# Performance work log

Measured on AMD Instinct MI355X. Metric: run time of the kernel, lower is better.

## Reference

```python
import jax, jax.numpy as jnp
import numpy as np

TOP_K = 2  # num_experts_per_tok


def setup_inputs() -> dict:
    key = jax.random.key(0)
    k1, k2, k3, k4, k5 = jax.random.split(key, 5)
    T, H, F, E = 2048, 2048, 1024, 8
    hidden_states = jax.random.normal(k1, (T, H), dtype=jnp.float32)
    router_logits = jax.random.normal(k2, (T, E), dtype=jnp.float32)
    s = 1.0 / np.sqrt(H)
    w1 = jax.random.normal(k3, (E, H, F), dtype=jnp.float32) * s  # gate proj
    w3 = jax.random.normal(k4, (E, H, F), dtype=jnp.float32) * s  # up proj
    w2 = jax.random.normal(k5, (E, F, H), dtype=jnp.float32) * (1.0 / np.sqrt(F))  # down proj
    return {"hidden_states": hidden_states, "router_logits": router_logits,
            "w1": w1, "w3": w3, "w2": w2}


def reference(hidden_states, router_logits, w1, w3, w2):
    # Top-K routing: softmax over raw logits, take top-k probs as combine weights
    # (renormalize_topk_logits=False, routed_scaling_factor=None).
    T, E = router_logits.shape
    probs = jax.nn.softmax(router_logits.astype(jnp.float32), axis=-1)  # (T, E)
    topk_w, topk_ids = jax.lax.top_k(probs, TOP_K)                      # (T, K)
    # Scatter combine weights into a dense (T, E) matrix (zeros off top-k).
    combine = jnp.zeros((T, E), dtype=probs.dtype).at[
        jnp.arange(T)[:, None], topk_ids].add(topk_w)                    # (T, E)

    x = hidden_states
    # SwiGLU expert FFN computed per-expert (dense over all tokens, masked by
    # combine weights -> same math as fused dispatch/grouped-GEMM/combine).
    g = jnp.einsum('th,ehf->etf', x, w1)          # (E, T, F) gate
    u = jnp.einsum('th,ehf->etf', x, w3)          # (E, T, F) up
    act = jax.nn.silu(g) * u                      # (E, T, F)
    act = act * combine.T[:, :, None]             # apply combine weight pre-down-proj
    y = jnp.einsum('etf,efh->th', act, w2)        # (T, H) combined over experts
    return y.astype(hidden_states.dtype)
```

## Files before the change

### kernel.cpp

```cpp
#include <hip/hip_runtime.h>
#include <stdint.h>

#define T_TOK 2048
#define HDIM  2048
#define FDIM  1024
#define NEXP  8

#define BM   128
#define BK   64
#define NTHR 256
#define MT_MAX 16
#define BN1  64
#define BN2  128
#define NT1 (FDIM / BN1)
#define NT2 (HDIM / BN2)
#define NK1 (HDIM / BK)
#define NK2 (FDIM / BK)
#define GRID1 (NEXP * MT_MAX * NT1)
#define GRID2 (NEXP * MT_MAX * NT2)
#define TILE_E 4096

typedef unsigned short u16;
typedef __attribute__((ext_vector_type(16))) float f32x16;
typedef __attribute__((ext_vector_type(8))) short bf16x8;

__device__ __forceinline__ u16 f2bf(float f) {
  uint32_t u = __float_as_uint(f);
  u += 0x7FFFu + ((u >> 16) & 1u);
  return (u16)(u >> 16);
}

__device__ __forceinline__ uint32_t pack2(float lo, float hi) {
  return (uint32_t)f2bf(lo) | ((uint32_t)f2bf(hi) << 16);
}

__device__ __forceinline__ void glds16(const u16* src, u16* dst) {
  __builtin_amdgcn_global_load_lds(
      (const __attribute__((address_space(1))) uint32_t*)src,
      (__attribute__((address_space(3))) uint32_t*)dst, 16, 0, 0);
}

__global__ void route1_kernel(const float* __restrict__ logits,
                              int* __restrict__ tok_e, float* __restrict__ tok_w,
                              int* __restrict__ counts) {
  __shared__ int lcnt[NEXP];
  const int tid = threadIdx.x;
  const int t = blockIdx.x * 256 + tid;
  if (tid < NEXP) lcnt[tid] = 0;
  __syncthreads();
  float l[NEXP];
#pragma unroll
  for (int e = 0; e < NEXP; ++e) l[e] = logits[t * NEXP + e];
  float m = l[0];
#pragma unroll
  for (int e = 1; e < NEXP; ++e) m = fmaxf(m, l[e]);
  float p[NEXP]; float s = 0.f;
#pragma unroll
  for (int e = 0; e < NEXP; ++e) { p[e] = __expf(l[e] - m); s += p[e]; }
  float inv = 1.f / s;
  int i0 = 0; float p0 = p[0];
#pragma unroll
  for (int e = 1; e < NEXP; ++e) if (p[e] > p0) { p0 = p[e]; i0 = e; }
  int i1 = -1; float p1 = -1.f;
#pragma unroll
  for (int e = 0; e < NEXP; ++e) if (e != i0 && p[e] > p1) { p1 = p[e]; i1 = e; }
  tok_e[t] = i0 | (i1 << 8);
  tok_w[t * 2]     = p0 * inv;
  tok_w[t * 2 + 1] = p1 * inv;
  atomicAdd(&lcnt[i0], 1);
  atomicAdd(&lcnt[i1], 1);
  __syncthreads();
  if (tid < NEXP) atomicAdd(&counts[tid], lcnt[tid]);
}

__global__ void route2_kernel(const int* __restrict__ counts,
                              int* __restrict__ offsets, int* __restrict__ cursor) {
  if (threadIdx.x == 0) {
    int s = 0;
    for (int e = 0; e < NEXP; ++e) { offsets[e] = s; cursor[e] = s; s += counts[e]; }
    offsets[NEXP] = s;
  }
}

__global__ void route3_kernel(const int* __restrict__ tok_e, const float* __restrict__ tok_w,
                              int* __restrict__ cursor,
                              int* __restrict__ token_list, float* __restrict__ slot_w) {
  __shared__ int lcnt[NEXP], lbase[NEXP];
  const int tid = threadIdx.x;
  const int t = blockIdx.x * 256 + tid;
  if (tid < NEXP) lcnt[tid] = 0;
  __syncthreads();
  int ee = tok_e[t];
  int e0 = ee & 255, e1 = ee >> 8;
  int li0 = atomicAdd(&lcnt[e0], 1);
  int li1 = atomicAdd(&lcnt[e1], 1);
  __syncthreads();
  if (tid < NEXP) lbase[tid] = atomicAdd(&cursor[tid], lcnt[tid]);
  __syncthreads();
  int s0 = lbase[e0] + li0;
  int s1 = lbase[e1] + li1;
  token_list[s0] = t; slot_w[s0] = tok_w[t * 2];
  token_list[s1] = t; slot_w[s1] = tok_w[t * 2 + 1];
}

__global__ void convert_x_kernel(const float4* __restrict__ x, ushort4* __restrict__ xb) {
  int i = blockIdx.x * 256 + threadIdx.x;
  float4 v = x[i];
  ushort4 o;
  o.x = f2bf(v.x); o.y = f2bf(v.y); o.z = f2bf(v.z); o.w = f2bf(v.w);
  xb[i] = o;
}

__global__ __launch_bounds__(256, 4)
void tconv_tiled_kernel(const float* __restrict__ w1, const float* __restrict__ w3,
                        const float* __restrict__ w2,
                        u16* __restrict__ w1b, u16* __restrict__ w3b, u16* __restrict__ w2b) {
  const int zb = blockIdx.y;
  const int which = zb >> 3;
  const int e = zb & 7;
  const int x = blockIdx.x;
  const float* src; u16* dstbase; int C, ct, ktg, NKT;
  if (which == 0)      { src = w1; dstbase = w1b; C = FDIM; ct = x & 15; ktg = x >> 4; NKT = 32; }
  else if (which == 1) { src = w3; dstbase = w3b; C = FDIM; ct = x & 15; ktg = x >> 4; NKT = 32; }
  else                 { src = w2; dstbase = w2b; C = HDIM; ct = x & 31; ktg = x >> 5; NKT = 16; }
  const size_t msz = (size_t)HDIM * FDIM;
  src += (size_t)e * msz;
  const int NTt = (which == 2) ? 32 : 16;
  u16* blob = dstbase + (((size_t)e * NTt + ct) * NKT + ktg * 4) * TILE_E;
  const int r0 = ktg * 256;
  const int c0 = ct * 64;

  __shared__ uint32_t T[4][64 * 33];
  const int t = threadIdx.x;

  const int kp = t >> 3;
  const int cg = t & 7;
  float4 a0[4], a1[4], b0[4], b1[4];
#pragma unroll
  for (int i = 0; i < 4; ++i) {
    const float* s0 = src + (size_t)(r0 + i * 64 + 2 * kp) * C + c0 + cg * 8;
    a0[i] = *(const float4*)(s0);
    a1[i] = *(const float4*)(s0 + 4);
    b0[i] = *(const float4*)(s0 + C);
    b1[i] = *(const float4*)(s0 + C + 4);
  }
#pragma unroll
  for (int i = 0; i < 4; ++i) {
    uint32_t* Ti = T[i];
    Ti[(cg * 8 + 0) * 33 + kp] = pack2(a0[i].x, b0[i].x);
    Ti[(cg * 8 + 1) * 33 + kp] = pack2(a0[i].y, b0[i].y);
    Ti[(cg * 8 + 2) * 33 + kp] = pack2(a0[i].z, b0[i].z);
    Ti[(cg * 8 + 3) * 33 + kp] = pack2(a0[i].w, b0[i].w);
    Ti[(cg * 8 + 4) * 33 + kp] = pack2(a1[i].x, b1[i].x);
    Ti[(cg * 8 + 5) * 33 + kp] = pack2(a1[i].y, b1[i].y);
    Ti[(cg * 8 + 6) * 33 + kp] = pack2(a1[i].z, b1[i].z);
    Ti[(cg * 8 + 7) * 33 + kp] = pack2(a1[i].w, b1[i].w);
  }
  __syncthreads();

  const int f  = t >> 2;
  const int kg = t & 3;
  const int swl = f & 7;
  uint32_t* bu = (uint32_t*)blob;
#pragma unroll
  for (int i = 0; i < 4; ++i) {
    const uint32_t* Ti = T[i] + f * 33 + kg * 8;
    uint4 q0 = {Ti[0], Ti[1], Ti[2], Ti[3]};
    uint4 q1 = {Ti[4], Ti[5], Ti[6], Ti[7]};
    uint32_t* br = bu + i * 2048 + f * 32;
    *(uint4*)(br + (((kg * 2) ^ swl) * 4))     = q0;
    *(uint4*)(br + (((kg * 2 + 1) ^ swl) * 4)) = q1;
  }
}

__global__ __launch_bounds__(NTHR, 3)
void gemm1_kernel(const u16* __restrict__ Xb,
                  const u16* __restrict__ w1b,
                  const u16* __restrict__ w3b,
                  const int* __restrict__ token_list,
                  const float* __restrict__ slot_w,
                  const int* __restrict__ counts,
                  const int* __restrict__ offsets,
                  u16* __restrict__ act) {
  const int bid = blockIdx.x;
  const int e  = bid >> 8;
  const int mt = (bid >> 4) & 15;
  const int nt = bid & 15;
  const int cnt = counts[e];
  if (mt * BM >= cnt) return;
  const int off = offsets[e];
  const int tid  = threadIdx.x;
  const int lane = tid & 63;
  const int wid  = tid >> 6;
  const int wr = wid >> 1;
  const int wc = wid & 1;

  __shared__ u16 A_lds[BM * BK];
  __shared__ u16 B1_lds[BN1 * BK];
  __shared__ u16 B3_lds[BN1 * BK];

  const u16* a_src[4];
#pragma unroll
  for (int i = 0; i < 4; ++i) {
    int row = (wid * 4 + i) * 8 + (lane >> 3);
    int mg = mt * BM + row;
    int mc = (mg < cnt) ? mg : (cnt - 1);
    int tok = token_list[off + mc];
    a_src[i] = Xb + (size_t)tok * HDIM + (((lane & 7) ^ (row & 7)) * 8);
  }
  const u16* b1_src[2];
  const u16* b3_src[2];
  {
    size_t tbase = ((size_t)(e * 16 + nt) * 32) * TILE_E;
#pragma unroll
    for (int i = 0; i < 2; ++i) {
      int c = wid * 2 + i;
      b1_src[i] = w1b + tbase + c * 512 + lane * 8;
      b3_src[i] = w3b + tbase + c * 512 + lane * 8;
    }
  }

  f32x16 accg[2] = {};
  f32x16 accu[2] = {};

#pragma unroll
  for (int i = 0; i < 4; ++i) glds16(a_src[i], &A_lds[(wid * 4 + i) * 512]);
#pragma unroll
  for (int i = 0; i < 2; ++i) {
    glds16(b1_src[i], &B1_lds[(wid * 2 + i) * 512]);
    glds16(b3_src[i], &B3_lds[(wid * 2 + i) * 512]);
  }

#pragma unroll 1
  for (int t = 0; t < NK1; ++t) {
    __syncthreads();
    bf16x8 af[2][4], bg[4], bu[4];
#pragma unroll
    for (int m = 0; m < 2; ++m) {
      int R = wr * 64 + m * 32 + (lane & 31);
#pragma unroll
      for (int kk = 0; kk < 4; ++kk) {
        int gl = kk * 2 + (lane >> 5);
        af[m][kk] = *(const bf16x8*)&A_lds[R * BK + ((gl ^ (R & 7)) * 8)];
      }
    }
    {
      int R = wc * 32 + (lane & 31);
#pragma unroll
      for (int kk = 0; kk < 4; ++kk) {
        int gl = kk * 2 + (lane >> 5);
        int pos = R * BK + ((gl ^ (R & 7)) * 8);
        bg[kk] = *(const bf16x8*)&B1_lds[pos];
        bu[kk] = *(const bf16x8*)&B3_lds[pos];
      }
    }
    __syncthreads();
    if (t + 1 < NK1) {
      const size_t ks = (size_t)(t + 1) * BK;
      const size_t kb = (size_t)(t + 1) * TILE_E;
#pragma unroll
      for (int i = 0; i < 4; ++i) glds16(a_src[i] + ks, &A_lds[(wid * 4 + i) * 512]);
#pragma unroll
      for (int i = 0; i < 2; ++i) {
        glds16(b1_src[i] + kb, &B1_lds[(wid * 2 + i) * 512]);
        glds16(b3_src[i] + kb, &B3_lds[(wid * 2 + i) * 512]);
      }
    }
#pragma unroll
    for (int m = 0; m < 2; ++m)
#pragma unroll
      for (int kk = 0; kk < 4; ++kk) {
        accg[m] = __builtin_amdgcn_mfma_f32_32x32x16_bf16(af[m][kk], bg[kk], accg[m], 0, 0, 0);
        accu[m] = __builtin_amdgcn_mfma_f32_32x32x16_bf16(af[m][kk], bu[kk], accu[m], 0, 0, 0);
      }
  }

  const int fcol = nt * BN1 + wc * 32 + (lane & 31);
#pragma unroll
  for (int m = 0; m < 2; ++m) {
    int base = mt * BM + wr * 64 + m * 32 + 4 * (lane >> 5);
#pragma unroll
    for (int reg = 0; reg < 16; ++reg) {
      int mg = base + (reg & 3) + 8 * (reg >> 2);
      if (mg < cnt) {
        int slot = off + mg;
        float wgt = slot_w[slot];
        float g = accg[m][reg];
        float u = accu[m][reg];
        float sv = g / (1.f + __expf(-g));
        act[(size_t)slot * FDIM + fcol] = f2bf(sv * u * wgt);
      }
    }
  }
}

__global__ __launch_bounds__(NTHR, 3)
void gemm2_kernel(const u16* __restrict__ act,
                  const u16* __restrict__ w2b,
                  const int* __restrict__ token_list,
                  const int* __restrict__ counts,
                  const int* __restrict__ offsets,
                  float* __restrict__ y) {
  const int bid = blockIdx.x;
  const int e  = bid >> 8;
  const int mt = (bid >> 4) & 15;
  const int nt = bid & 15;
  const int cnt = counts[e];
  if (mt * BM >= cnt) return;
  const int off = offsets[e];
  const int tid  = threadIdx.x;
  const int lane = tid & 63;
  const int wid  = tid >> 6;
  const int wr = wid >> 1;
  const int wc = wid & 1;

  __shared__ u16 A_lds[BM * BK];
  __shared__ u16 B_lds[BN2 * BK];

  const u16* a_src[4];
  const u16* b_src[4];
#pragma unroll
  for (int i = 0; i < 4; ++i) {
    int row = (wid * 4 + i) * 8 + (lane >> 3);
    int mg = mt * BM + row;
    int mc = (mg < cnt) ? mg : (cnt - 1);
    a_src[i] = act + (size_t)(off + mc) * FDIM + (((lane & 7) ^ (row & 7)) * 8);
    int c = wid * 4 + i;
    size_t tbase = ((size_t)(e * 32 + nt * 2 + (c >> 3)) * 16) * TILE_E;
    b_src[i] = w2b + tbase + (c & 7) * 512 + lane * 8;
  }

  f32x16 acc[2][2] = {};

#pragma unroll
  for (int i = 0; i < 4; ++i) {
    glds16(a_src[i], &A_lds[(wid * 4 + i) * 512]);
    glds16(b_src[i], &B_lds[(wid * 4 + i) * 512]);
  }

#pragma unroll 1
  for (int t = 0; t < NK2; ++t) {
    __syncthreads();
    bf16x8 af[2][4], bb[2][4];
#pragma unroll
    for (int m = 0; m < 2; ++m) {
      int R = wr * 64 + m * 32 + (lane & 31);
#pragma unroll
      for (int kk = 0; kk < 4; ++kk) {
        int gl = kk * 2 + (lane >> 5);
        af[m][kk] = *(const bf16x8*)&A_lds[R * BK + ((gl ^ (R & 7)) * 8)];
      }
    }
#pragma unroll
    for (int n = 0; n < 2; ++n) {
      int R = wc * 64 + n * 32 + (lane & 31);
#pragma unroll
      for (int kk = 0; kk < 4; ++kk) {
        int gl = kk * 2 + (lane >> 5);
        bb[n][kk] = *(const bf16x8*)&B_lds[R * BK + ((gl ^ (R & 7)) * 8)];
      }
    }
    __syncthreads();
    if (t + 1 < NK2) {
      const size_t ks = (size_t)(t + 1) * BK;
      const size_t kb = (size_t)(t + 1) * TILE_E;
#pragma unroll
      for (int i = 0; i < 4; ++i) {
        glds16(a_src[i] + ks, &A_lds[(wid * 4 + i) * 512]);
        glds16(b_src[i] + kb, &B_lds[(wid * 4 + i) * 512]);
      }
    }
#pragma unroll
    for (int kk = 0; kk < 4; ++kk)
#pragma unroll
      for (int m = 0; m < 2; ++m)
#pragma unroll
        for (int n = 0; n < 2; ++n)
          acc[m][n] = __builtin_amdgcn_mfma_f32_32x32x16_bf16(af[m][kk], bb[n][kk], acc[m][n], 0, 0, 0);
  }

#pragma unroll
  for (int m = 0; m < 2; ++m) {
    int base = mt * BM + wr * 64 + m * 32 + 4 * (lane >> 5);
#pragma unroll
    for (int reg = 0; reg < 16; ++reg) {
      int mg = base + (reg & 3) + 8 * (reg >> 2);
      if (mg < cnt) {
        int slot = off + mg;
        int tok = token_list[slot];
#pragma unroll
        for (int n = 0; n < 2; ++n) {
          int hcol = nt * BN2 + wc * 64 + n * 32 + (lane & 31);
          unsafeAtomicAdd(y + (size_t)tok * HDIM + hcol, acc[m][n][reg]);
        }
      }
    }
  }
}

extern "C" void kernel_launch(void* const* d_in, const int* in_sizes, int n_in,
                              void* d_out, int out_size, void* d_ws, size_t ws_size,
                              hipStream_t stream) {
  (void)in_sizes; (void)n_in; (void)out_size; (void)ws_size;
  const float* hs     = (const float*)d_in[0];
  const float* logits = (const float*)d_in[1];
  const float* w1     = (const float*)d_in[2];
  const float* w3     = (const float*)d_in[3];
  const float* w2     = (const float*)d_in[4];
  float* y = (float*)d_out;

  uint8_t* ws = (uint8_t*)d_ws;
  int*   token_list = (int*)(ws);
  float* slot_w     = (float*)(ws + (16 << 10));
  int*   counts     = (int*)(ws + (32 << 10));
  int*   offsets    = (int*)(ws + (32 << 10) + 128);
  int*   cursor     = (int*)(ws + (32 << 10) + 256);
  int*   tok_e      = (int*)(ws + (33 << 10));
  float* tok_w      = (float*)(ws + (42 << 10));
  const size_t MB = 1 << 20;
  u16*   Xb  = (u16*)(ws + (64 << 10));
  u16*   act = (u16*)(ws + (64 << 10) + 8 * MB);
  u16*   w1b = (u16*)(ws + (64 << 10) + 16 * MB);
  u16*   w3b = (u16*)(ws + (64 << 10) + 48 * MB);
  u16*   w2b = (u16*)(ws + (64 << 10) + 80 * MB);

  hipMemsetAsync(counts, 0, NEXP * sizeof(int), stream);
  route1_kernel<<<T_TOK / 256, 256, 0, stream>>>(logits, tok_e, tok_w, counts);
  route2_kernel<<<1, 64, 0, stream>>>(counts, offsets, cursor);
  route3_kernel<<<T_TOK / 256, 256, 0, stream>>>(tok_e, tok_w, cursor, token_list, slot_w);
  convert_x_kernel<<<(T_TOK * HDIM / 4) / 256, 256, 0, stream>>>((const float4*)hs, (ushort4*)Xb);
  tconv_tiled_kernel<<<dim3(128, 24), 256, 0, stream>>>(w1, w3, w2, w1b, w3b, w2b);
  hipMemsetAsync(d_out, 0, (size_t)T_TOK * HDIM * sizeof(float), stream);
  gemm1_kernel<<<GRID1, NTHR, 0, stream>>>(Xb, w1b, w3b, token_list, slot_w, counts, offsets, act);
  gemm2_kernel<<<GRID2, NTHR, 0, stream>>>(act, w2b, token_list, counts, offsets, y);
}
```

Before: 182.0 us.

## Fuse weight conversion, input cast and output zeroing into combined launches

Merges the w1/w3 bf16 conversion, the hidden-state cast and the output zeroing into one kernel, and runs the w2 conversion inside the gemm1 launch so it overlaps with gemm1 compute. The weight tile layout changes to a smaller swizzle, and the LDS read addressing in both GEMMs is updated to match. The aim is fewer launches and overlap of the memory-bound conversion with compute. The cost is a different LDS swizzle that may add bank conflicts, and the gemm1 blocks now share occupancy with the conversion blocks.

```diff
diff --git a/kernel.cpp b/kernel.cpp
--- a/kernel.cpp
+++ b/kernel.cpp
@@ -16,9 +16,9 @@
 #define NT2 (HDIM / BN2)
 #define NK1 (HDIM / BK)
 #define NK2 (FDIM / BK)
-#define GRID1 (NEXP * MT_MAX * NT1)
-#define GRID2 (NEXP * MT_MAX * NT2)
+#define GRID2K (NEXP * MT_MAX * NT2)
 #define TILE_E 4096
+#define SMEM_BYTES 36864
 
 typedef unsigned short u16;
 typedef __attribute__((ext_vector_type(16))) float f32x16;
@@ -103,89 +103,102 @@
   token_list[s1] = t; slot_w[s1] = tok_w[t * 2 + 1];
 }
 
-__global__ void convert_x_kernel(const float4* __restrict__ x, ushort4* __restrict__ xb) {
-  int i = blockIdx.x * 256 + threadIdx.x;
-  float4 v = x[i];
-  ushort4 o;
-  o.x = f2bf(v.x); o.y = f2bf(v.y); o.z = f2bf(v.z); o.w = f2bf(v.w);
-  xb[i] = o;
-}
-
-__global__ __launch_bounds__(256, 4)
-void tconv_tiled_kernel(const float* __restrict__ w1, const float* __restrict__ w3,
-                        const float* __restrict__ w2,
-                        u16* __restrict__ w1b, u16* __restrict__ w3b, u16* __restrict__ w2b) {
-  const int zb = blockIdx.y;
-  const int which = zb >> 3;
-  const int e = zb & 7;
-  const int x = blockIdx.x;
-  const float* src; u16* dstbase; int C, ct, ktg, NKT;
-  if (which == 0)      { src = w1; dstbase = w1b; C = FDIM; ct = x & 15; ktg = x >> 4; NKT = 32; }
-  else if (which == 1) { src = w3; dstbase = w3b; C = FDIM; ct = x & 15; ktg = x >> 4; NKT = 32; }
-  else                 { src = w2; dstbase = w2b; C = HDIM; ct = x & 31; ktg = x >> 5; NKT = 16; }
-  const size_t msz = (size_t)HDIM * FDIM;
-  src += (size_t)e * msz;
-  const int NTt = (which == 2) ? 32 : 16;
-  u16* blob = dstbase + (((size_t)e * NTt + ct) * NKT + ktg * 4) * TILE_E;
-  const int r0 = ktg * 256;
-  const int c0 = ct * 64;
-
-  __shared__ uint32_t T[4][64 * 33];
+__device__ __forceinline__ void wconv_block(const float* __restrict__ src,
+                                            u16* __restrict__ dstb,
+                                            int C, int NT, int NKT,
+                                            int e, int r0, int c0, uint32_t* L) {
   const int t = threadIdx.x;
-
-  const int kp = t >> 3;
-  const int cg = t & 7;
-  float4 a0[4], a1[4], b0[4], b1[4];
+  const int p  = t >> 5;
+  const int ln = t & 31;
+  const float* row0 = src + (size_t)(r0 + 2 * p) * C + c0;
+  const float* row1 = row0 + C;
+  float4 f0[8], f1[8];
+#pragma unroll
+  for (int j = 0; j < 8; ++j) f0[j] = *(const float4*)(row0 + j * 128 + ln * 4);
+#pragma unroll
+  for (int j = 0; j < 8; ++j) f1[j] = *(const float4*)(row1 + j * 128 + ln * 4);
+#pragma unroll
+  for (int j = 0; j < 8; ++j) {
+    int n = j * 128 + ln * 4;
+    L[(n + 0) * 9 + p] = pack2(f0[j].x, f1[j].x);
+    L[(n + 1) * 9 + p] = pack2(f0[j].y, f1[j].y);
+    L[(n + 2) * 9 + p] = pack2(f0[j].z, f1[j].z);
+    L[(n + 3) * 9 + p] = pack2(f0[j].w, f1[j].w);
+  }
+  __syncthreads();
+  const int kt = r0 >> 6, kq = (r0 >> 4) & 3;
 #pragma unroll
   for (int i = 0; i < 4; ++i) {
-    const float* s0 = src + (size_t)(r0 + i * 64 + 2 * kp) * C + c0 + cg * 8;
-    a0[i] = *(const float4*)(s0);
-    a1[i] = *(const float4*)(s0 + 4);
-    b0[i] = *(const float4*)(s0 + C);
-    b1[i] = *(const float4*)(s0 + C + 4);
-  }
-#pragma unroll
-  for (int i = 0; i < 4; ++i) {
-    uint32_t* Ti = T[i];
-    Ti[(cg * 8 + 0) * 33 + kp] = pack2(a0[i].x, b0[i].x);
-    Ti[(cg * 8 + 1) * 33 + kp] = pack2(a0[i].y, b0[i].y);
-    Ti[(cg * 8 + 2) * 33 + kp] = pack2(a0[i].z, b0[i].z);
-    Ti[(cg * 8 + 3) * 33 + kp] = pack2(a0[i].w, b0[i].w);
-    Ti[(cg * 8 + 4) * 33 + kp] = pack2(a1[i].x, b1[i].x);
-    Ti[(cg * 8 + 5) * 33 + kp] = pack2(a1[i].y, b1[i].y);
-    Ti[(cg * 8 + 6) * 33 + kp] = pack2(a1[i].z, b1[i].z);
-    Ti[(cg * 8 + 7) * 33 + kp] = pack2(a1[i].w, b1[i].w);
-  }
-  __syncthreads();
-
-  const int f  = t >> 2;
-  const int kg = t & 3;
-  const int swl = f & 7;
-  uint32_t* bu = (uint32_t*)blob;
-#pragma unroll
-  for (int i = 0; i < 4; ++i) {
-    const uint32_t* Ti = T[i] + f * 33 + kg * 8;
-    uint4 q0 = {Ti[0], Ti[1], Ti[2], Ti[3]};
-    uint4 q1 = {Ti[4], Ti[5], Ti[6], Ti[7]};
-    uint32_t* br = bu + i * 2048 + f * 32;
-    *(uint4*)(br + (((kg * 2) ^ swl) * 4))     = q0;
-    *(uint4*)(br + (((kg * 2 + 1) ^ swl) * 4)) = q1;
-  }
-}
-
-__global__ __launch_bounds__(NTHR, 3)
-void gemm1_kernel(const u16* __restrict__ Xb,
-                  const u16* __restrict__ w1b,
-                  const u16* __restrict__ w3b,
+    int n = t * 4 + i;
+    const uint32_t* a = &L[n * 9];
+    uint4 lo = {a[0], a[1], a[2], a[3]};
+    uint4 hi = {a[4], a[5], a[6], a[7]};
+    int ng = c0 + n;
+    int s = (n >> 2) & 1;
+    u16* tb = dstb + (((size_t)e * NT + (ng >> 6)) * NKT + kt) * TILE_E
+                   + kq * 1024 + (n & 63) * 16;
+    *(uint4*)(tb + s * 8)       = lo;
+    *(uint4*)(tb + (s ^ 1) * 8) = hi;
+  }
+}
+
+__global__ __launch_bounds__(256, 3)
+void mega1_kernel(const float* __restrict__ w1, const float* __restrict__ w3,
+                  u16* __restrict__ w1b, u16* __restrict__ w3b,
+                  const float4* __restrict__ x, ushort4* __restrict__ xb,
+                  float4* __restrict__ y4) {
+  __shared__ __align__(16) uint8_t smem[SMEM_BYTES];
+  const int bid = blockIdx.x;
+  const int t = threadIdx.x;
+  if (bid < 2048) {
+    const int m = bid >> 10;
+    const int r = bid & 1023;
+    const int e = r >> 7;
+    const int g = r & 127;
+    const size_t msz = (size_t)HDIM * FDIM;
+    wconv_block((m ? w3 : w1) + (size_t)e * msz, m ? w3b : w1b,
+                FDIM, 16, 32, e, g * 16, 0, (uint32_t*)smem);
+  } else if (bid < 2304) {
+    int i = (bid - 2048) * 256 + t;
+#pragma unroll
+    for (int r = 0; r < 16; ++r, i += 65536) {
+      float4 v = x[i];
+      ushort4 o;
+      o.x = f2bf(v.x); o.y = f2bf(v.y); o.z = f2bf(v.z); o.w = f2bf(v.w);
+      xb[i] = o;
+    }
+  } else {
+    int i = (bid - 2304) * 256 + t;
+    float4 z = {0.f, 0.f, 0.f, 0.f};
+#pragma unroll
+    for (int r = 0; r < 16; ++r, i += 65536) y4[i] = z;
+  }
+}
+
+__global__ __launch_bounds__(256, 3)
+void mega2_kernel(const float* __restrict__ w2, u16* __restrict__ w2b,
+                  const u16* __restrict__ Xb,
+                  const u16* __restrict__ w1b, const u16* __restrict__ w3b,
                   const int* __restrict__ token_list,
                   const float* __restrict__ slot_w,
                   const int* __restrict__ counts,
                   const int* __restrict__ offsets,
                   u16* __restrict__ act) {
+  __shared__ __align__(16) uint8_t smem[SMEM_BYTES];
   const int bid = blockIdx.x;
-  const int e  = bid >> 8;
-  const int mt = (bid >> 4) & 15;
-  const int nt = bid & 15;
+  if (bid < 1024) {
+    const int e = bid >> 7;
+    const int r = bid & 127;
+    const int g = r & 63;
+    const int half = r >> 6;
+    wconv_block(w2 + (size_t)e * HDIM * FDIM, w2b,
+                HDIM, 32, 16, e, g * 16, half * 1024, (uint32_t*)smem);
+    return;
+  }
+  const int gb = bid - 1024;
+  const int e  = gb >> 8;
+  const int mt = (gb >> 4) & 15;
+  const int nt = gb & 15;
   const int cnt = counts[e];
   if (mt * BM >= cnt) return;
   const int off = offsets[e];
@@ -195,9 +208,9 @@
   const int wr = wid >> 1;
   const int wc = wid & 1;
 
-  __shared__ u16 A_lds[BM * BK];
-  __shared__ u16 B1_lds[BN1 * BK];
-  __shared__ u16 B3_lds[BN1 * BK];
+  u16* A_lds  = (u16*)smem;
+  u16* B1_lds = (u16*)(smem + 16384);
+  u16* B3_lds = (u16*)(smem + 24576);
 
   const u16* a_src[4];
 #pragma unroll
@@ -246,12 +259,11 @@
     }
     {
       int R = wc * 32 + (lane & 31);
+      int base = R * 16 + (((lane >> 5) ^ ((R >> 2) & 1)) * 8);
 #pragma unroll
       for (int kk = 0; kk < 4; ++kk) {
-        int gl = kk * 2 + (lane >> 5);
-        int pos = R * BK + ((gl ^ (R & 7)) * 8);
-        bg[kk] = *(const bf16x8*)&B1_lds[pos];
-        bu[kk] = *(const bf16x8*)&B3_lds[pos];
+        bg[kk] = *(const bf16x8*)&B1_lds[base + kk * 1024];
+        bu[kk] = *(const bf16x8*)&B3_lds[base + kk * 1024];
       }
     }
     __syncthreads();
@@ -354,11 +366,10 @@
 #pragma unroll
     for (int n = 0; n < 2; ++n) {
       int R = wc * 64 + n * 32 + (lane & 31);
-#pragma unroll
-      for (int kk = 0; kk < 4; ++kk) {
-        int gl = kk * 2 + (lane >> 5);
-        bb[n][kk] = *(const bf16x8*)&B_lds[R * BK + ((gl ^ (R & 7)) * 8)];
-      }
+      int base = (R >> 6) * TILE_E + (R & 63) * 16 + (((lane >> 5) ^ ((R >> 2) & 1)) * 8);
+#pragma unroll
+      for (int kk = 0; kk < 4; ++kk)
+        bb[n][kk] = *(const bf16x8*)&B_lds[base + kk * 1024];
     }
     __syncthreads();
     if (t + 1 < NK2) {
@@ -428,9 +439,9 @@
   route1_kernel<<<T_TOK / 256, 256, 0, stream>>>(logits, tok_e, tok_w, counts);
   route2_kernel<<<1, 64, 0, stream>>>(counts, offsets, cursor);
   route3_kernel<<<T_TOK / 256, 256, 0, stream>>>(tok_e, tok_w, cursor, token_list, slot_w);
-  convert_x_kernel<<<(T_TOK * HDIM / 4) / 256, 256, 0, stream>>>((const float4*)hs, (ushort4*)Xb);
-  tconv_tiled_kernel<<<dim3(128, 24), 256, 0, stream>>>(w1, w3, w2, w1b, w3b, w2b);
-  hipMemsetAsync(d_out, 0, (size_t)T_TOK * HDIM * sizeof(float), stream);
-  gemm1_kernel<<<GRID1, NTHR, 0, stream>>>(Xb, w1b, w3b, token_list, slot_w, counts, offsets, act);
-  gemm2_kernel<<<GRID2, NTHR, 0, stream>>>(act, w2b, token_list, counts, offsets, y);
-}
+  mega1_kernel<<<2560, 256, 0, stream>>>(w1, w3, w1b, w3b,
+                                         (const float4*)hs, (ushort4*)Xb, (float4*)y);
+  mega2_kernel<<<3072, 256, 0, stream>>>(w2, w2b, Xb, w1b, w3b,
+                                         token_list, slot_w, counts, offsets, act);
+  gemm2_kernel<<<GRID2K, NTHR, 0, stream>>>(act, w2b, token_list, counts, offsets, y);
+}
```

Result: no change. 181.9 us (-0.1%).
